# Kernel tuning notes

Measured on AMD Instinct MI355X. Metric: run time of the kernel, lower is better.

The kernel has to match this reference:

```python
import jax, jax.numpy as jnp
import numpy as np


def setup_inputs() -> dict:
    key = jax.random.key(0)
    k1, k2 = jax.random.split(key)
    B, N = 2, 8192
    pred = jax.random.normal(k1, (B, N, 3), dtype=jnp.float32)
    gt = jax.random.normal(k2, (B, N, 3), dtype=jnp.float32)
    return {"pred": pred, "gt": gt}


def reference(pred, gt):
    # dist[b, i, j] = ||pred[b, j] - gt[b, i]||_2, computed via the
    # squared-norm expansion to avoid materializing a [B,N,N,3] diff tensor.
    p_sq = jnp.sum(pred * pred, axis=-1)  # [B, N]
    g_sq = jnp.sum(gt * gt, axis=-1)      # [B, N]
    # inner[b, i, j] = gt[b, i] . pred[b, j]
    inner = jnp.einsum("bid,bjd->bij", gt, pred)  # [B, N, N]
    sq_dist = g_sq[:, :, None] + p_sq[:, None, :] - 2.0 * inner
    dist = jnp.sqrt(jnp.maximum(sq_dist, 0.0))    # [B, N, N]
    dist1 = jnp.min(dist, axis=2)  # per-gt nearest pred distance, [B, N]
    dist2 = jnp.min(dist, axis=1)  # per-pred nearest gt distance, [B, N]
    chamfer = (dist1.mean(axis=1) + dist2.mean(axis=1)).mean()
    return chamfer
```

## Files before the change

kernel.cpp:

```cpp
#include <hip/hip_runtime.h>
#include <math.h>

#define NPTS  8192
#define BATCH 2
#define CJ    256
#define IPT   4
#define TPB   256
#define NSLOT (2 * BATCH * NPTS)
#define GX    (NSLOT / (TPB * IPT))
#define GY    (NPTS / CJ)

typedef float v2f __attribute__((ext_vector_type(2)));

__global__ __launch_bounds__(TPB) void chamfer_pairs(
    const float* __restrict__ pred, const float* __restrict__ gt,
    unsigned int* __restrict__ mins)
{
    __shared__ float xs[CJ], ys[CJ], zs[CJ], qs[CJ];

    const int base  = blockIdx.x * (TPB * IPT);
    const int dir   = base >> 14;
    const int b     = (base >> 13) & 1;
    const int ibase = base & (NPTS - 1);

    const float* pts  = (dir == 0 ? gt : pred) + (size_t)b * NPTS * 3;
    const float* cand = (dir == 0 ? pred : gt) + (size_t)b * NPTS * 3;

    const int j0 = blockIdx.y * CJ;
    for (int jj = threadIdx.x; jj < CJ; jj += TPB) {
        float x = cand[(size_t)(j0 + jj) * 3 + 0];
        float y = cand[(size_t)(j0 + jj) * 3 + 1];
        float z = cand[(size_t)(j0 + jj) * 3 + 2];
        xs[jj] = x; ys[jj] = y; zs[jj] = z;
        qs[jj] = 0.5f * (x * x + y * y + z * z);
    }

    float px[IPT], py[IPT], pz[IPT];
    v2f   m2[IPT];
#pragma unroll
    for (int k = 0; k < IPT; ++k) {
        int i = ibase + threadIdx.x + k * TPB;
        px[k] = pts[(size_t)i * 3 + 0];
        py[k] = pts[(size_t)i * 3 + 1];
        pz[k] = pts[(size_t)i * 3 + 2];
        m2[k] = (v2f)(3.0e38f);
    }
    __syncthreads();

    const v2f* xs2 = (const v2f*)xs;
    const v2f* ys2 = (const v2f*)ys;
    const v2f* zs2 = (const v2f*)zs;
    const v2f* qs2 = (const v2f*)qs;

#pragma unroll 8
    for (int j = 0; j < CJ / 2; ++j) {
        v2f cx = xs2[j], cy = ys2[j], cz = zs2[j], cq = qs2[j];
#pragma unroll
        for (int k = 0; k < IPT; ++k) {
            v2f t = cq - cx * px[k];
            t = t - cy * py[k];
            t = t - cz * pz[k];
            m2[k].x = fminf(m2[k].x, t.x);
            m2[k].y = fminf(m2[k].y, t.y);
        }
    }

#pragma unroll
    for (int k = 0; k < IPT; ++k) {
        float gsq = fmaf(px[k], px[k], fmaf(py[k], py[k], pz[k] * pz[k]));
        float t   = fminf(m2[k].x, m2[k].y);
        float d2  = fmaxf(fmaf(2.0f, t, gsq), 0.0f);
        atomicMin(&mins[base + k * TPB + threadIdx.x], __float_as_uint(d2));
    }
}

__global__ __launch_bounds__(1024) void chamfer_reduce(
    const unsigned int* __restrict__ mins, float* __restrict__ out)
{
    float s = 0.f;
#pragma unroll
    for (int r = 0; r < NSLOT / 1024; ++r)
        s += sqrtf(__uint_as_float(mins[r * 1024 + threadIdx.x]));

    for (int off = 32; off > 0; off >>= 1)
        s += __shfl_down(s, off, 64);

    __shared__ float ws[16];
    const int wave = threadIdx.x >> 6, lane = threadIdx.x & 63;
    if (lane == 0) ws[wave] = s;
    __syncthreads();
    if (threadIdx.x == 0) {
        float t = 0.f;
#pragma unroll
        for (int w = 0; w < 16; ++w) t += ws[w];
        out[0] = t * (1.0f / (float)(BATCH * NPTS));
    }
}

extern "C" void kernel_launch(void* const* d_in, const int* in_sizes, int n_in,
                              void* d_out, int out_size, void* d_ws, size_t ws_size,
                              hipStream_t stream) {
    const float* pred = (const float*)d_in[0];
    const float* gt   = (const float*)d_in[1];
    unsigned int* mins = (unsigned int*)d_ws;

    dim3 grid(GX, GY);
    chamfer_pairs<<<grid, TPB, 0, stream>>>(pred, gt, mins);
    chamfer_reduce<<<1, 1024, 0, stream>>>(mins, (float*)d_out);
}
```

Measured before the change: 79.83 us.

## Use packed FMA and min3 inline asm with more points per thread

The inner distance loop now uses explicit v_pk_fma_f32 with pre-negated, pre-broadcast query coordinates, and merges the two running minima into one with v_min3_f32. This cuts VALU instructions per pair. Points per thread rise from 4 to 8 and the candidate tile shrinks to 128, giving 64 column blocks, so each shared-memory load is reused across more points. The cost is higher register pressure and fewer row blocks, with more atomicMin traffic per slot.

```diff
diff --git a/kernel.cpp b/kernel.cpp
--- a/kernel.cpp
+++ b/kernel.cpp
@@ -3,14 +3,25 @@
 
 #define NPTS  8192
 #define BATCH 2
-#define CJ    256
-#define IPT   4
+#define GY    64
+#define CJ    (NPTS / GY)
+#define IPT   8
 #define TPB   256
 #define NSLOT (2 * BATCH * NPTS)
 #define GX    (NSLOT / (TPB * IPT))
-#define GY    (NPTS / CJ)
 
 typedef float v2f __attribute__((ext_vector_type(2)));
+
+static __device__ __forceinline__ v2f pk_fma(v2f a, v2f b, v2f c) {
+    v2f d;
+    asm("v_pk_fma_f32 %0, %1, %2, %3" : "=v"(d) : "v"(a), "v"(b), "v"(c));
+    return d;
+}
+static __device__ __forceinline__ float min3(float a, float b, float c) {
+    float d;
+    asm("v_min3_f32 %0, %1, %2, %3" : "=v"(d) : "v"(a), "v"(b), "v"(c));
+    return d;
+}
 
 __global__ __launch_bounds__(TPB) void chamfer_pairs(
     const float* __restrict__ pred, const float* __restrict__ gt,
@@ -27,7 +38,8 @@
     const float* cand = (dir == 0 ? pred : gt) + (size_t)b * NPTS * 3;
 
     const int j0 = blockIdx.y * CJ;
-    for (int jj = threadIdx.x; jj < CJ; jj += TPB) {
+    if (threadIdx.x < CJ) {
+        int jj = threadIdx.x;
         float x = cand[(size_t)(j0 + jj) * 3 + 0];
         float y = cand[(size_t)(j0 + jj) * 3 + 1];
         float z = cand[(size_t)(j0 + jj) * 3 + 2];
@@ -35,15 +47,18 @@
         qs[jj] = 0.5f * (x * x + y * y + z * z);
     }
 
-    float px[IPT], py[IPT], pz[IPT];
-    v2f   m2[IPT];
+    float px[IPT], py[IPT], pz[IPT], m[IPT];
+    v2f npx2[IPT], npy2[IPT], npz2[IPT];
 #pragma unroll
     for (int k = 0; k < IPT; ++k) {
         int i = ibase + threadIdx.x + k * TPB;
         px[k] = pts[(size_t)i * 3 + 0];
         py[k] = pts[(size_t)i * 3 + 1];
         pz[k] = pts[(size_t)i * 3 + 2];
-        m2[k] = (v2f)(3.0e38f);
+        npx2[k] = (v2f)(-px[k]);
+        npy2[k] = (v2f)(-py[k]);
+        npz2[k] = (v2f)(-pz[k]);
+        m[k]  = 3.0e38f;
     }
     __syncthreads();
 
@@ -52,24 +67,22 @@
     const v2f* zs2 = (const v2f*)zs;
     const v2f* qs2 = (const v2f*)qs;
 
-#pragma unroll 8
+#pragma unroll 4
     for (int j = 0; j < CJ / 2; ++j) {
         v2f cx = xs2[j], cy = ys2[j], cz = zs2[j], cq = qs2[j];
 #pragma unroll
         for (int k = 0; k < IPT; ++k) {
-            v2f t = cq - cx * px[k];
-            t = t - cy * py[k];
-            t = t - cz * pz[k];
-            m2[k].x = fminf(m2[k].x, t.x);
-            m2[k].y = fminf(m2[k].y, t.y);
+            v2f t = pk_fma(cx, npx2[k], cq);
+            t = pk_fma(cy, npy2[k], t);
+            t = pk_fma(cz, npz2[k], t);
+            m[k] = min3(m[k], t.x, t.y);
         }
     }
 
 #pragma unroll
     for (int k = 0; k < IPT; ++k) {
         float gsq = fmaf(px[k], px[k], fmaf(py[k], py[k], pz[k] * pz[k]));
-        float t   = fminf(m2[k].x, m2[k].y);
-        float d2  = fmaxf(fmaf(2.0f, t, gsq), 0.0f);
+        float d2  = fmaxf(fmaf(2.0f, m[k], gsq), 0.0f);
         atomicMin(&mins[base + k * TPB + threadIdx.x], __float_as_uint(d2));
     }
 }
```

Result: no change. 81.34 us (+1.9%).
